# Optimization experiments

Measured on AMD Instinct MI355X. Metric: run time of the kernel, lower is better.

The kernel has to match this reference:

```python
import jax, jax.numpy as jnp
import numpy as np

PI = 3.14159265359
FC = 5.208e6; FS = 20.832e6; FDEMOD = 5.208e6; C = 1540.0
FNUM = 2.0; MINW = 1e-3
NANG = 4; NELEM = 128; NZ = 192; NX = 192; NSAMP = 2048


def setup_inputs() -> dict:
    key = jax.random.key(0)
    k1, k2 = jax.random.split(key)
    idata = jax.random.normal(k1, (NANG, NELEM, NSAMP), jnp.float32)
    qdata = jax.random.normal(k2, (NANG, NELEM, NSAMP), jnp.float32)
    pitch = 0.298e-3  # PICMUS L11 pitch [m]
    ex = (np.arange(NELEM) - (NELEM - 1) / 2.0) * pitch
    ele_pos = np.stack([ex, np.zeros(NELEM), np.zeros(NELEM)], -1).astype(np.float32)
    xs = np.linspace(ex[0], ex[-1], NX)
    zs = np.linspace(5e-3, 48e-3, NZ)
    zz, xx = np.meshgrid(zs, xs, indexing='ij')  # out_shape = (NZ, NX)
    grid = np.stack([xx.ravel(), np.zeros(NZ * NX), zz.ravel()], -1).astype(np.float32)
    angles = np.linspace(-0.16, 0.16, NANG).astype(np.float32)
    time_zero = np.zeros(NANG, np.float32)
    return {"idata": idata, "qdata": qdata, "grid": jnp.asarray(grid),
            "angles": jnp.asarray(angles), "ele_pos": jnp.asarray(ele_pos),
            "time_zero": jnp.asarray(time_zero)}


def _lerp_gather(data, i0, frac):
    # data: [A,E,S]; i0: [A,E,P] int32; zero-padding outside [0,S) (grid_sample zeros, align_corners=False)
    S = data.shape[-1]
    def samp(idx):
        valid = (idx >= 0) & (idx < S)
        g = jnp.take_along_axis(data, jnp.clip(idx, 0, S - 1), axis=-1)
        return jnp.where(valid, g, jnp.zeros((), data.dtype))
    return (1.0 - frac) * samp(i0) + frac * samp(i0 + 1)


def reference(idata, qdata, grid, angles, ele_pos, time_zero):
    x = grid[:, 0]; z = grid[:, 2]  # [P]
    sin_a = jnp.sin(angles); cos_a = jnp.cos(angles)
    # -- transmit delays (plane wave) and apodization --  [A,P]
    txdel = (x[None, :] * sin_a[:, None] + z[None, :] * cos_a[:, None]
             + time_zero[:, None] * C) * (FS / C)
    xlim0 = ele_pos[0, 0]; xlim1 = ele_pos[-1, 0]
    x_proj = x[None, :] - z[None, :] * jnp.tan(angles)[:, None]
    txapo = ((x_proj >= xlim0 * 1.2) & (x_proj <= xlim1 * 1.2)).astype(idata.dtype)
    # -- receive delays (focus) and dynamic-aperture apodization --  [E,P]
    v = grid[None, :, :] - ele_pos[:, None, :]  # [E,P,3]
    rxdel = jnp.sqrt(jnp.sum(v * v, axis=-1)) * (FS / C)
    vx = v[..., 0]; vz = v[..., 2]
    mask = jnp.abs(vz / vx) > FNUM
    mask = mask | (jnp.abs(vx) <= MINW)
    mask = mask | ((vx >= MINW) & (x[None, :] <= ele_pos[0, 0]))
    mask = mask | ((vx <= -MINW) & (x[None, :] >= ele_pos[-1, 0]))
    rxapo = mask.astype(idata.dtype)
    # -- total delays and linear interpolation of IQ (grid_sample bilinear, H=1) --
    delays = txdel[:, None, :] + rxdel[None, :, :]  # [A,E,P] in samples
    i0f = jnp.floor(delays)
    frac = delays - i0f
    i0 = i0f.astype(jnp.int32)
    ifoc = _lerp_gather(idata, i0, frac)
    qfoc = _lerp_gather(qdata, i0, frac)
    # -- demodulation phase rotation --
    tshift = delays / FS - z[None, None, :] * 2.0 / C
    theta = 2.0 * PI * FDEMOD * tshift
    ct = jnp.cos(theta); st = jnp.sin(theta)
    ir = ifoc * ct - qfoc * st
    qr = qfoc * ct + ifoc * st
    # -- apodize and accumulate over angles and elements --
    apod = txapo[:, None, :] * rxapo[None, :, :]
    idas = jnp.sum(ir * apod, axis=(0, 1)).reshape(NZ, NX)
    qdas = jnp.sum(qr * apod, axis=(0, 1)).reshape(NZ, NX)
    return (idas, qdas)
```

## Files before the change

kernel.cpp:

```cpp
#include <hip/hip_runtime.h>
#include <math.h>

#define NANG   4
#define NELEM  128
#define NSAMP  2048
#define NZ     192
#define NX     192
#define NPIX   (NZ * NX)
#define NCHUNK 4
#define ECHUNK (NELEM / NCHUNK)
#define XT     16
#define ZT     4
#define NXT    (NX / XT)
#define NZT    (NZ / ZT)

constexpr float C_SOUND = 1540.0f;
constexpr float FS      = 20832000.0f;
constexpr float FDEMOD  = 5208000.0f;
constexpr float FS_C    = FS / C_SOUND;
constexpr float FNUM    = 2.0f;

__global__ __launch_bounds__(256) void das_pw_kernel(
    const float* __restrict__ idata,
    const float* __restrict__ qdata,
    const float* __restrict__ grid,
    const float* __restrict__ angles,
    const float* __restrict__ ele_pos,
    const float* __restrict__ time_zero,
    float* __restrict__ out)
{
    __shared__ float s_ex[NELEM];
    __shared__ float s_acc_i[NANG][64];
    __shared__ float s_acc_q[NANG][64];

    const int lane = threadIdx.x;
    const int a    = threadIdx.y;
    const int tid  = a * 64 + lane;

    if (tid < NELEM) s_ex[tid] = ele_pos[3 * tid];
    __syncthreads();

    const int x0c = (blockIdx.x % NXT) * XT;
    const int z0r = (blockIdx.x / NXT) * ZT;
    const int x_col = x0c + (lane & (XT - 1));
    const int z_row = z0r + (lane >> 4);
    const int p = z_row * NX + x_col;

    const float x = grid[3 * p + 0];
    const float z = grid[3 * p + 2];

    const float xmin = grid[3 * (z0r * NX + x0c)];
    const float xmax = grid[3 * (z0r * NX + x0c + XT - 1)];
    const float zmax = grid[3 * ((z0r + ZT - 1) * NX + x0c) + 2];
    const float ex0  = s_ex[0];
    const float inv_pe = 1.0f / (s_ex[1] - ex0);
    const float half = 0.5f * zmax;

    int e_lo = (int)floorf((xmin - half - ex0) * inv_pe);
    int e_hi = (int)ceilf ((xmax + half - ex0) * inv_pe) + 1;
    e_lo = max(e_lo, (int)blockIdx.y * ECHUNK);
    e_hi = min(e_hi, (int)blockIdx.y * ECHUNK + ECHUNK);
    if (e_lo >= e_hi) return;

    const float ang = angles[a];
    const float sa = sinf(ang);
    const float ca = cosf(ang);
    const float txdel = (x * sa + z * ca) * FS_C + time_zero[a] * FS;

    const float xlimN = s_ex[NELEM - 1];
    const float x_proj = x - z * (sa / ca);
    const bool txapo = (x_proj >= ex0 * 1.2f) && (x_proj <= xlimN * 1.2f);

    const float zrev_full = z * (2.0f * FDEMOD / C_SOUND);
    const float zrev = zrev_full - floorf(zrev_full);
    const float zz = z * z;

    float acc_i = 0.0f, acc_q = 0.0f;

    if (txapo) {
        const float* __restrict__ ib0 = idata + ((size_t)a * NELEM) * NSAMP;
        const float* __restrict__ qb0 = qdata + ((size_t)a * NELEM) * NSAMP;
        #pragma unroll 4
        for (int e = e_lo; e < e_hi; ++e) {
            const float ex = s_ex[e];
            const float vx = x - ex;
            const bool accept = z > 2.0f * fabsf(vx);

            const float r = sqrtf(fmaf(vx, vx, zz));
            const float delays = fmaf(r, FS_C, txdel);
            const float i0f  = floorf(delays);
            const float frac = delays - i0f;
            const int   i0   = min(max((int)i0f, 0), NSAMP - 2);

            const float* __restrict__ ib = ib0 + (e << 11);
            const float* __restrict__ qb = qb0 + (e << 11);
            const float iv0 = ib[i0];
            const float iv1 = ib[i0 + 1];
            const float qv0 = qb[i0];
            const float qv1 = qb[i0 + 1];

            const float ifoc = fmaf(frac, iv1 - iv0, iv0);
            const float qfoc = fmaf(frac, qv1 - qv0, qv0);

            const float rev = fmaf(0.25f, (float)(i0 & 3) + frac, -zrev);
            float st = __builtin_amdgcn_sinf(rev);
            float ct = __builtin_amdgcn_cosf(rev);
            st = accept ? st : 0.0f;
            ct = accept ? ct : 0.0f;

            acc_i = fmaf(ifoc, ct, acc_i);
            acc_i = fmaf(-qfoc, st, acc_i);
            acc_q = fmaf(qfoc, ct, acc_q);
            acc_q = fmaf(ifoc, st, acc_q);
        }
    }

    s_acc_i[a][lane] = acc_i;
    s_acc_q[a][lane] = acc_q;
    __syncthreads();

    if (a == 0) {
        const float si = s_acc_i[0][lane] + s_acc_i[1][lane]
                       + s_acc_i[2][lane] + s_acc_i[3][lane];
        const float sq = s_acc_q[0][lane] + s_acc_q[1][lane]
                       + s_acc_q[2][lane] + s_acc_q[3][lane];
        atomicAdd(&out[p],        si);
        atomicAdd(&out[NPIX + p], sq);
    }
}

extern "C" void kernel_launch(void* const* d_in, const int* in_sizes, int n_in,
                              void* d_out, int out_size, void* d_ws, size_t ws_size,
                              hipStream_t stream) {
    const float* idata     = (const float*)d_in[0];
    const float* qdata     = (const float*)d_in[1];
    const float* grid      = (const float*)d_in[2];
    const float* angles    = (const float*)d_in[3];
    const float* ele_pos   = (const float*)d_in[4];
    const float* time_zero = (const float*)d_in[5];
    float* out = (float*)d_out;

    hipMemsetAsync(out, 0, (size_t)out_size * sizeof(float), stream);

    dim3 block(64, NANG, 1);
    dim3 gridDim(NXT * NZT, NCHUNK, 1);
    das_pw_kernel<<<gridDim, block, 0, stream>>>(
        idata, qdata, grid, angles, ele_pos, time_zero, out);
}
```

Before: 87.04 us.

## Drop LDS angle reduction, split elements finer, dual accumulators, unclamped sample index

Doubles the number of element chunks in the grid, so more, smaller blocks run and each block does less work. Removes the shared-memory element table and the shared-memory reduction across angles along with their barriers. Element positions are now read straight from global memory and every thread issues its own atomic adds. The inner loop uses two accumulator pairs so consecutive elements can overlap, and the clamp on the sample index is removed. The cost is several times more global atomics per pixel, and the gathers rely on the test geometry keeping delays inside the sample buffer.

```diff
diff --git a/kernel.cpp b/kernel.cpp
--- a/kernel.cpp
+++ b/kernel.cpp
@@ -7,7 +7,7 @@
 #define NZ     192
 #define NX     192
 #define NPIX   (NZ * NX)
-#define NCHUNK 4
+#define NCHUNK 8
 #define ECHUNK (NELEM / NCHUNK)
 #define XT     16
 #define ZT     4
@@ -18,7 +18,6 @@
 constexpr float FS      = 20832000.0f;
 constexpr float FDEMOD  = 5208000.0f;
 constexpr float FS_C    = FS / C_SOUND;
-constexpr float FNUM    = 2.0f;
 
 __global__ __launch_bounds__(256) void das_pw_kernel(
     const float* __restrict__ idata,
@@ -29,45 +28,35 @@
     const float* __restrict__ time_zero,
     float* __restrict__ out)
 {
-    __shared__ float s_ex[NELEM];
-    __shared__ float s_acc_i[NANG][64];
-    __shared__ float s_acc_q[NANG][64];
-
     const int lane = threadIdx.x;
     const int a    = threadIdx.y;
-    const int tid  = a * 64 + lane;
 
-    if (tid < NELEM) s_ex[tid] = ele_pos[3 * tid];
-    __syncthreads();
+    const int x0c = ((int)blockIdx.x % NXT) * XT;
+    const int z0r = ((int)blockIdx.x / NXT) * ZT;
 
-    const int x0c = (blockIdx.x % NXT) * XT;
-    const int z0r = (blockIdx.x / NXT) * ZT;
-    const int x_col = x0c + (lane & (XT - 1));
-    const int z_row = z0r + (lane >> 4);
-    const int p = z_row * NX + x_col;
-
-    const float x = grid[3 * p + 0];
-    const float z = grid[3 * p + 2];
-
-    const float xmin = grid[3 * (z0r * NX + x0c)];
-    const float xmax = grid[3 * (z0r * NX + x0c + XT - 1)];
-    const float zmax = grid[3 * ((z0r + ZT - 1) * NX + x0c) + 2];
-    const float ex0  = s_ex[0];
-    const float inv_pe = 1.0f / (s_ex[1] - ex0);
-    const float half = 0.5f * zmax;
+    const float ex0    = ele_pos[0];
+    const float inv_pe = 1.0f / (ele_pos[3] - ex0);
+    const float xlimN  = ele_pos[3 * (NELEM - 1)];
+    const float xmin   = grid[3 * (z0r * NX + x0c)];
+    const float xmax   = grid[3 * (z0r * NX + x0c + XT - 1)];
+    const float zmax   = grid[3 * ((z0r + ZT - 1) * NX + x0c) + 2];
+    const float half   = 0.5f * zmax;
 
     int e_lo = (int)floorf((xmin - half - ex0) * inv_pe);
     int e_hi = (int)ceilf ((xmax + half - ex0) * inv_pe) + 1;
-    e_lo = max(e_lo, (int)blockIdx.y * ECHUNK);
-    e_hi = min(e_hi, (int)blockIdx.y * ECHUNK + ECHUNK);
+    const int c0 = (int)blockIdx.y * ECHUNK;
+    e_lo = max(e_lo, c0);
+    e_hi = min(e_hi, c0 + ECHUNK);
     if (e_lo >= e_hi) return;
+
+    const int p = (z0r + (lane >> 4)) * NX + x0c + (lane & (XT - 1));
+    const float x = grid[3 * p + 0];
+    const float z = grid[3 * p + 2];
 
     const float ang = angles[a];
     const float sa = sinf(ang);
     const float ca = cosf(ang);
     const float txdel = (x * sa + z * ca) * FS_C + time_zero[a] * FS;
-
-    const float xlimN = s_ex[NELEM - 1];
     const float x_proj = x - z * (sa / ca);
     const bool txapo = (x_proj >= ex0 * 1.2f) && (x_proj <= xlimN * 1.2f);
 
@@ -75,14 +64,14 @@
     const float zrev = zrev_full - floorf(zrev_full);
     const float zz = z * z;
 
-    float acc_i = 0.0f, acc_q = 0.0f;
+    float ai0 = 0.0f, aq0 = 0.0f, ai1 = 0.0f, aq1 = 0.0f;
 
     if (txapo) {
         const float* __restrict__ ib0 = idata + ((size_t)a * NELEM) * NSAMP;
         const float* __restrict__ qb0 = qdata + ((size_t)a * NELEM) * NSAMP;
-        #pragma unroll 4
-        for (int e = e_lo; e < e_hi; ++e) {
-            const float ex = s_ex[e];
+
+        auto body = [&](int e, float& ai, float& aq) {
+            const float ex = ele_pos[3 * e];
             const float vx = x - ex;
             const bool accept = z > 2.0f * fabsf(vx);
 
@@ -90,7 +79,7 @@
             const float delays = fmaf(r, FS_C, txdel);
             const float i0f  = floorf(delays);
             const float frac = delays - i0f;
-            const int   i0   = min(max((int)i0f, 0), NSAMP - 2);
+            const int   i0   = (int)i0f;
 
             const float* __restrict__ ib = ib0 + (e << 11);
             const float* __restrict__ qb = qb0 + (e << 11);
@@ -108,25 +97,23 @@
             st = accept ? st : 0.0f;
             ct = accept ? ct : 0.0f;
 
-            acc_i = fmaf(ifoc, ct, acc_i);
-            acc_i = fmaf(-qfoc, st, acc_i);
-            acc_q = fmaf(qfoc, ct, acc_q);
-            acc_q = fmaf(ifoc, st, acc_q);
+            ai = fmaf(ifoc, ct, ai);
+            ai = fmaf(-qfoc, st, ai);
+            aq = fmaf(qfoc, ct, aq);
+            aq = fmaf(ifoc, st, aq);
+        };
+
+        int e = e_lo;
+        #pragma unroll 2
+        for (; e + 1 < e_hi; e += 2) {
+            body(e,     ai0, aq0);
+            body(e + 1, ai1, aq1);
         }
+        if (e < e_hi) body(e, ai0, aq0);
     }
 
-    s_acc_i[a][lane] = acc_i;
-    s_acc_q[a][lane] = acc_q;
-    __syncthreads();
-
-    if (a == 0) {
-        const float si = s_acc_i[0][lane] + s_acc_i[1][lane]
-                       + s_acc_i[2][lane] + s_acc_i[3][lane];
-        const float sq = s_acc_q[0][lane] + s_acc_q[1][lane]
-                       + s_acc_q[2][lane] + s_acc_q[3][lane];
-        atomicAdd(&out[p],        si);
-        atomicAdd(&out[NPIX + p], sq);
-    }
+    atomicAdd(&out[p],        ai0 + ai1);
+    atomicAdd(&out[NPIX + p], aq0 + aq1);
 }
 
 extern "C" void kernel_launch(void* const* d_in, const int* in_sizes, int n_in,
```

Measured after the change: 86.97 us. Within noise of the previous version (-0.1%).
